# Kernel tuning notes

Measured on AMD Instinct MI355X. Metric: run time of the kernel, lower is better.

The kernel has to match this reference:

```python
import jax, jax.numpy as jnp
import numpy as np

N = 50000
E = 800000
B = 8  # number of graphs


def gcn_conv(x, src, dst, W, b, n_nodes):
    # PyG GCNConv: add self-loops, symmetric deg^{-1/2} normalization,
    # linear transform, scatter-add aggregation at dst, then bias.
    loops = jnp.arange(n_nodes, dtype=src.dtype)
    s = jnp.concatenate([src, loops])
    d = jnp.concatenate([dst, loops])
    deg = jax.ops.segment_sum(jnp.ones_like(d, dtype=x.dtype), d, num_segments=n_nodes)
    dinv = jnp.where(deg > 0, jax.lax.rsqrt(deg), 0.0)
    norm = dinv[s] * dinv[d]                      # [E+N]
    xw = x @ W                                    # [N, out]
    msg = xw[s] * norm[:, None]                   # gather + scale
    out = jax.ops.segment_sum(msg, d, num_segments=n_nodes)  # scatter-add
    return out + b


def global_attention(x, batch, gate_w, gate_b, n_graphs):
    gate = x @ gate_w + gate_b                    # [N, 1]
    gmax = jax.ops.segment_max(gate, batch, num_segments=n_graphs)
    gmax = jnp.where(jnp.isfinite(gmax), gmax, 0.0)
    e = jnp.exp(gate - gmax[batch])               # segment-stable softmax
    denom = jax.ops.segment_sum(e, batch, num_segments=n_graphs)
    alpha = e / denom[batch]                      # [N, 1]
    return jax.ops.segment_sum(alpha * x, batch, num_segments=n_graphs)  # [B, d]


def setup_inputs() -> dict:
    key = jax.random.key(0)
    ks = jax.random.split(key, 10)
    x = jax.random.normal(ks[0], (N, 512), dtype=jnp.float32)
    edge_index = jax.random.randint(ks[1], (2, E), 0, N, dtype=jnp.int32)
    batch = jnp.sort(jax.random.randint(ks[2], (N,), 0, B, dtype=jnp.int32))
    W1 = jax.random.normal(ks[3], (512, 256), dtype=jnp.float32) / np.sqrt(512)
    b1 = jnp.zeros((256,), dtype=jnp.float32)
    W2 = jax.random.normal(ks[4], (256, 256), dtype=jnp.float32) / np.sqrt(256)
    b2 = jnp.zeros((256,), dtype=jnp.float32)
    gate_w = jax.random.normal(ks[5], (256, 1), dtype=jnp.float32) / np.sqrt(256)
    gate_b = jnp.zeros((1,), dtype=jnp.float32)
    return {"x": x, "edge_index": edge_index, "batch": batch,
            "W1": W1, "b1": b1, "W2": W2, "b2": b2,
            "gate_w": gate_w, "gate_b": gate_b}


def reference(x, edge_index, batch, W1, b1, W2, b2, gate_w, gate_b):
    src, dst = edge_index[0], edge_index[1]
    h = jax.nn.relu(gcn_conv(x, src, dst, W1, b1, N))
    h = jax.nn.relu(gcn_conv(h, src, dst, W2, b2, N))
    return global_attention(h, batch, gate_w, gate_b, B)
```

## Files before the change

kernel.cpp:

```cpp
#include <hip/hip_runtime.h>
#include <hip/hip_bf16.h>
#include <math.h>

#define FDIM 256
#define CAP 64
#define NGRAPH 8
#define GMAX_BLOCKS 64
#define FINAL_BLOCKS 512

typedef __attribute__((ext_vector_type(8))) short bf16x8;
typedef __attribute__((ext_vector_type(4))) float f32x4;

__device__ __forceinline__ unsigned enc_f(float x){
  unsigned u = __float_as_uint(x);
  return (u >> 31) ? ~u : (u | 0x80000000u);
}
__device__ __forceinline__ float dec_f(unsigned u){
  return (u >> 31) ? __uint_as_float(u & 0x7FFFFFFFu) : __uint_as_float(~u);
}

__device__ __forceinline__ unsigned short f2bf(float f){
  unsigned u = __float_as_uint(f);
  unsigned r = (u + 0x7FFFu + ((u >> 16) & 1u)) >> 16;
  return (unsigned short)r;
}
__device__ __forceinline__ float bf2f(unsigned short h){
  return __uint_as_float(((unsigned)h) << 16);
}
__device__ __forceinline__ unsigned pk2(float a, float b){
  return (unsigned)f2bf(a) | ((unsigned)f2bf(b) << 16);
}

__global__ void init_k(int* cnt, float* denom, float* out, int N){
  int i = blockIdx.x * blockDim.x + threadIdx.x;
  if (i < N) cnt[i] = 0;
  if (i < NGRAPH) denom[i] = 0.f;
  if (i < NGRAPH * FDIM) out[i] = 0.f;
}

__global__ void csr_k(const int* __restrict__ src, const int* __restrict__ dst,
                      int* __restrict__ cnt, int* __restrict__ col, int E){
  int e = blockIdx.x * blockDim.x + threadIdx.x;
  if (e < E){
    int d = dst[e];
    int pos = atomicAdd(&cnt[d], 1);
    if (pos < CAP) col[(size_t)d * CAP + pos] = src[e];
  }
}

__global__ void dinv_k(const int* __restrict__ cnt, float* __restrict__ dinv, int N){
  int i = blockIdx.x * blockDim.x + threadIdx.x;
  if (i < N) dinv[i] = rsqrtf((float)(cnt[i] + 1));
}

template<int K>
__global__ void wconv_k(const float* __restrict__ W, unsigned short* __restrict__ Wt){
  int idx = blockIdx.x * 256 + threadIdx.x;
  if (idx >= K * 256) return;
  int k = idx >> 8, n = idx & 255;
  Wt[(size_t)n * K + k] = f2bf(W[idx]);
}

template<int K, bool A_FP32>
__global__ __launch_bounds__(512) void gemm_k(const void* __restrict__ Av,
                                              const unsigned short* __restrict__ Bt,
                                              unsigned short* __restrict__ C, int M){
  __shared__ unsigned short As[128 * 64];
  __shared__ unsigned short Bs[256 * 64];
  const int tid = threadIdx.x;
  const int lane = tid & 63, wid = tid >> 6;
  const int wr = wid >> 2, wc = wid & 3;
  const int m0 = blockIdx.x * 128;
  f32x4 acc[4][4] = {};

  float4 arf0, arf1, arf2, arf3;
  uint4  arb0, arb1;
  uint4  brg0, brg1, brg2, brg3;

  const int rA0 = tid >> 3,          kqA0 = tid & 7;
  const int rA1 = (512 + tid) >> 3,  kqA1 = tid & 7;

  auto issue = [&](int k0){
    if (A_FP32){
      const float* A = (const float*)Av;
      const float* p0 = A + (size_t)min(m0 + rA0, M - 1) * K + k0 + kqA0 * 8;
      const float* p1 = A + (size_t)min(m0 + rA1, M - 1) * K + k0 + kqA1 * 8;
      arf0 = *(const float4*)p0; arf1 = *(const float4*)(p0 + 4);
      arf2 = *(const float4*)p1; arf3 = *(const float4*)(p1 + 4);
    } else {
      const unsigned short* A = (const unsigned short*)Av;
      arb0 = *(const uint4*)(A + (size_t)min(m0 + rA0, M - 1) * K + k0 + kqA0 * 8);
      arb1 = *(const uint4*)(A + (size_t)min(m0 + rA1, M - 1) * K + k0 + kqA1 * 8);
    }
    {
      int n0 = tid >> 3, n1 = (512 + tid) >> 3, n2 = (1024 + tid) >> 3, n3 = (1536 + tid) >> 3;
      int kq = tid & 7;
      brg0 = *(const uint4*)(Bt + (size_t)n0 * K + k0 + kq * 8);
      brg1 = *(const uint4*)(Bt + (size_t)n1 * K + k0 + kq * 8);
      brg2 = *(const uint4*)(Bt + (size_t)n2 * K + k0 + kq * 8);
      brg3 = *(const uint4*)(Bt + (size_t)n3 * K + k0 + kq * 8);
    }
  };

  auto writeLDS = [&](){
    int kq = tid & 7;
    {
      uint4 u0, u1;
      if (A_FP32){
        u0.x = pk2(arf0.x, arf0.y); u0.y = pk2(arf0.z, arf0.w);
        u0.z = pk2(arf1.x, arf1.y); u0.w = pk2(arf1.z, arf1.w);
        u1.x = pk2(arf2.x, arf2.y); u1.y = pk2(arf2.z, arf2.w);
        u1.z = pk2(arf3.x, arf3.y); u1.w = pk2(arf3.z, arf3.w);
      } else { u0 = arb0; u1 = arb1; }
      *(uint4*)((char*)As + ((rA0 * 128 + kq * 16) ^ ((rA0 & 7) << 4))) = u0;
      *(uint4*)((char*)As + ((rA1 * 128 + kq * 16) ^ ((rA1 & 7) << 4))) = u1;
    }
    {
      int n0 = tid >> 3, n1 = (512 + tid) >> 3, n2 = (1024 + tid) >> 3, n3 = (1536 + tid) >> 3;
      *(uint4*)((char*)Bs + ((n0 * 128 + kq * 16) ^ ((n0 & 7) << 4))) = brg0;
      *(uint4*)((char*)Bs + ((n1 * 128 + kq * 16) ^ ((n1 & 7) << 4))) = brg1;
      *(uint4*)((char*)Bs + ((n2 * 128 + kq * 16) ^ ((n2 & 7) << 4))) = brg2;
      *(uint4*)((char*)Bs + ((n3 * 128 + kq * 16) ^ ((n3 & 7) << 4))) = brg3;
    }
  };

  issue(0);
  for (int k0 = 0; k0 < K; k0 += 64){
    writeLDS();
    __syncthreads();
    if (k0 + 64 < K) issue(k0 + 64);

    #pragma unroll
    for (int kk = 0; kk < 64; kk += 32){
      bf16x8 af[4], bfr[4];
      int kb = kk * 2 + ((lane >> 4) << 4);
      #pragma unroll
      for (int mi = 0; mi < 4; ++mi){
        int r = wr * 64 + mi * 16 + (lane & 15);
        af[mi] = *(bf16x8*)((char*)As + ((r * 128 + kb) ^ ((r & 7) << 4)));
      }
      #pragma unroll
      for (int ni = 0; ni < 4; ++ni){
        int n = wc * 64 + ni * 16 + (lane & 15);
        bfr[ni] = *(bf16x8*)((char*)Bs + ((n * 128 + kb) ^ ((n & 7) << 4)));
      }
      #pragma unroll
      for (int mi = 0; mi < 4; ++mi)
        #pragma unroll
        for (int ni = 0; ni < 4; ++ni)
          acc[mi][ni] = __builtin_amdgcn_mfma_f32_16x16x32_bf16(af[mi], bfr[ni], acc[mi][ni], 0, 0, 0);
    }
    __syncthreads();
  }

  #pragma unroll
  for (int mi = 0; mi < 4; ++mi){
    #pragma unroll
    for (int reg = 0; reg < 4; ++reg){
      int row = m0 + wr * 64 + mi * 16 + ((lane >> 4) << 2) + reg;
      if (row < M){
        #pragma unroll
        for (int ni = 0; ni < 4; ++ni){
          int colc = wc * 64 + ni * 16 + (lane & 15);
          C[(size_t)row * FDIM + colc] = f2bf(acc[mi][ni][reg]);
        }
      }
    }
  }
}

template<bool OUT_BF16, bool GATE>
__global__ __launch_bounds__(64) void agg_k(const unsigned short* __restrict__ xw,
                                            const float* __restrict__ dinv,
                                            const int* __restrict__ col,
                                            const int* __restrict__ cnt,
                                            const float* __restrict__ bias,
                                            void* __restrict__ outv,
                                            const float* __restrict__ gw,
                                            const float* __restrict__ gb,
                                            float* __restrict__ gate, int N){
  int i = blockIdx.x;
  int lane = threadIdx.x;
  float di = dinv[i];
  int n = min(cnt[i], CAP);
  int s = 0; float w = 0.f;
  if (lane < n){ s = col[(size_t)i * CAP + lane]; w = di * dinv[s]; }

  float a0, a1, a2, a3;
  {
    ushort4 v = *(const ushort4*)(xw + (size_t)i * FDIM + lane * 4);
    float sw = di * di;
    a0 = sw * bf2f(v.x); a1 = sw * bf2f(v.y); a2 = sw * bf2f(v.z); a3 = sw * bf2f(v.w);
  }

  uint2 bufA[8], bufB[8];
  int nc = (n + 7) >> 3;

  auto loadChunk = [&](uint2 (&buf)[8], int c){
    #pragma unroll
    for (int j = 0; j < 8; ++j){
      int e = c * 8 + j;
      int se = __shfl(s, e);
      buf[j] = *(const uint2*)(xw + (size_t)se * FDIM + lane * 4);
    }
  };
  auto consChunk = [&](uint2 (&buf)[8], int c){
    #pragma unroll
    for (int j = 0; j < 8; ++j){
      int e = c * 8 + j;
      float we = __shfl(w, e);
      ushort4 v = *(ushort4*)&buf[j];
      a0 += we * bf2f(v.x); a1 += we * bf2f(v.y);
      a2 += we * bf2f(v.z); a3 += we * bf2f(v.w);
    }
  };

  if (nc > 0) loadChunk(bufA, 0);
  for (int c = 0; c < nc; ++c){
    if (c & 1){
      if (c + 1 < nc) loadChunk(bufA, c + 1);
      consChunk(bufB, c);
    } else {
      if (c + 1 < nc) loadChunk(bufB, c + 1);
      consChunk(bufA, c);
    }
  }

  float4 bv = *(const float4*)(bias + lane * 4);
  a0 = fmaxf(a0 + bv.x, 0.f); a1 = fmaxf(a1 + bv.y, 0.f);
  a2 = fmaxf(a2 + bv.z, 0.f); a3 = fmaxf(a3 + bv.w, 0.f);
  if (OUT_BF16){
    ushort4 r = make_ushort4(f2bf(a0), f2bf(a1), f2bf(a2), f2bf(a3));
    *(ushort4*)((unsigned short*)outv + (size_t)i * FDIM + lane * 4) = r;
  } else {
    *(float4*)((float*)outv + (size_t)i * FDIM + lane * 4) = make_float4(a0, a1, a2, a3);
  }
  if (GATE){
    float4 g = *(const float4*)(gw + lane * 4);
    float val = a0 * g.x + a1 * g.y + a2 * g.z + a3 * g.w;
    #pragma unroll
    for (int off = 32; off; off >>= 1) val += __shfl_down(val, off);
    if (lane == 0) gate[i] = val + gb[0];
  }
}

__global__ __launch_bounds__(256) void gmax_k(const float* __restrict__ gate,
                                              const int* __restrict__ batch,
                                              unsigned* __restrict__ pmax, int N){
  __shared__ unsigned smax[NGRAPH];
  int tid = threadIdx.x;
  if (tid < NGRAPH) smax[tid] = 0u;
  __syncthreads();
  int chunk = (N + gridDim.x - 1) / gridDim.x;
  int begin = blockIdx.x * chunk;
  int end = min(begin + chunk, N);
  int curg = -1; unsigned curm = 0u;
  for (int i = begin + tid; i < end; i += 256){
    int g = batch[i];
    unsigned v = enc_f(gate[i]);
    if (g != curg){
      if (curg >= 0) atomicMax(&smax[curg], curm);
      curg = g; curm = v;
    } else if (v > curm) curm = v;
  }
  if (curg >= 0) atomicMax(&smax[curg], curm);
  __syncthreads();
  if (tid < NGRAPH) pmax[blockIdx.x * NGRAPH + tid] = smax[tid];
}

__global__ __launch_bounds__(256) void denom_k(float* __restrict__ gate,
                                               const int* __restrict__ batch,
                                               const unsigned* __restrict__ pmax,
                                               float* __restrict__ denom, int N){
  __shared__ unsigned sge[NGRAPH];
  __shared__ float gm[NGRAPH];
  __shared__ float dsum[NGRAPH];
  int tid = threadIdx.x;
  if (tid < NGRAPH){ sge[tid] = 0u; dsum[tid] = 0.f; }
  __syncthreads();
  for (int j = tid; j < GMAX_BLOCKS * NGRAPH; j += 256)
    atomicMax(&sge[j & (NGRAPH - 1)], pmax[j]);
  __syncthreads();
  if (tid < NGRAPH){
    unsigned u = sge[tid];
    gm[tid] = (u == 0u) ? 0.f : dec_f(u);
  }
  __syncthreads();
  int chunk = (N + gridDim.x - 1) / gridDim.x;
  int begin = blockIdx.x * chunk;
  int end = min(begin + chunk, N);
  int curg = -1; float cursum = 0.f;
  for (int i = begin + tid; i < end; i += 256){
    int g = batch[i];
    float e = expf(gate[i] - gm[g]);
    gate[i] = e;
    if (g != curg){
      if (curg >= 0) atomicAdd(&dsum[curg], cursum);
      curg = g; cursum = e;
    } else cursum += e;
  }
  if (curg >= 0) atomicAdd(&dsum[curg], cursum);
  __syncthreads();
  if (tid < NGRAPH && dsum[tid] != 0.f) atomicAdd(&denom[tid], dsum[tid]);
}

__global__ __launch_bounds__(256) void final_k(const float* __restrict__ h,
                                               const float* __restrict__ e,
                                               const int* __restrict__ batch,
                                               const float* __restrict__ denom,
                                               float* __restrict__ out, int N){
  __shared__ float sacc[NGRAPH * FDIM];
  int tid = threadIdx.x;
  #pragma unroll
  for (int j = tid; j < NGRAPH * FDIM; j += 256) sacc[j] = 0.f;
  __syncthreads();
  int lane = tid & 63, w = tid >> 6;
  int chunk = (N + gridDim.x - 1) / gridDim.x;
  int begin = blockIdx.x * chunk;
  int end = min(begin + chunk, N);
  float4 acc = make_float4(0.f, 0.f, 0.f, 0.f);
  int curg = -1;
  for (int i = begin + w; i < end; i += 4){
    int g = batch[i];
    if (g != curg){
      if (curg >= 0){
        atomicAdd(&sacc[curg * FDIM + lane * 4 + 0], acc.x);
        atomicAdd(&sacc[curg * FDIM + lane * 4 + 1], acc.y);
        atomicAdd(&sacc[curg * FDIM + lane * 4 + 2], acc.z);
        atomicAdd(&sacc[curg * FDIM + lane * 4 + 3], acc.w);
        acc = make_float4(0.f, 0.f, 0.f, 0.f);
      }
      curg = g;
    }
    float alpha = e[i] / denom[g];
    float4 v = *(const float4*)(h + (size_t)i * FDIM + lane * 4);
    acc.x += alpha * v.x; acc.y += alpha * v.y;
    acc.z += alpha * v.z; acc.w += alpha * v.w;
  }
  if (curg >= 0){
    atomicAdd(&sacc[curg * FDIM + lane * 4 + 0], acc.x);
    atomicAdd(&sacc[curg * FDIM + lane * 4 + 1], acc.y);
    atomicAdd(&sacc[curg * FDIM + lane * 4 + 2], acc.z);
    atomicAdd(&sacc[curg * FDIM + lane * 4 + 3], acc.w);
  }
  __syncthreads();
  if (begin < end){
    int g0 = batch[begin], g1 = batch[end - 1];
    for (int g = g0; g <= g1; ++g){
      float v = sacc[g * FDIM + tid];
      if (v != 0.f) atomicAdd(&out[g * FDIM + tid], v);
    }
  }
}

extern "C" void kernel_launch(void* const* d_in, const int* in_sizes, int n_in,
                              void* d_out, int out_size, void* d_ws, size_t ws_size,
                              hipStream_t stream){
  const float* x     = (const float*)d_in[0];
  const int*   ei    = (const int*)  d_in[1];
  const int*   batch = (const int*)  d_in[2];
  const float* W1    = (const float*)d_in[3];
  const float* b1    = (const float*)d_in[4];
  const float* W2    = (const float*)d_in[5];
  const float* b2    = (const float*)d_in[6];
  const float* gw    = (const float*)d_in[7];
  const float* gb    = (const float*)d_in[8];
  float* out = (float*)d_out;

  const int N = in_sizes[2];
  const int E = in_sizes[1] / 2;
  const int* src = ei;
  const int* dst = ei + E;

  size_t off = 0;
  auto carve = [&](size_t bytes) -> void* {
    void* p = (char*)d_ws + off;
    off += (bytes + 255) / 256 * 256;
    return p;
  };
  float*          h     = (float*)         carve((size_t)N * FDIM * 4);
  unsigned short* h1b   = (unsigned short*)carve((size_t)N * FDIM * 2);
  unsigned short* xwb   = (unsigned short*)carve((size_t)N * FDIM * 2);
  int*            cnt   = (int*)           carve((size_t)N * 4);
  float*          dinv  = (float*)         carve((size_t)N * 4);
  int*            col   = (int*)           carve((size_t)N * CAP * 4);
  float*          gate  = (float*)         carve((size_t)N * 4);
  unsigned*       pmax  = (unsigned*)      carve(GMAX_BLOCKS * NGRAPH * 4);
  float*          denom = (float*)         carve(NGRAPH * 4);
  unsigned short* Wt1   = (unsigned short*)carve((size_t)256 * 512 * 2);
  unsigned short* Wt2   = (unsigned short*)carve((size_t)256 * 256 * 2);
  (void)ws_size; (void)n_in; (void)out_size;

  const int TB = 256;
  init_k<<<(N + TB - 1) / TB, TB, 0, stream>>>(cnt, denom, out, N);
  csr_k<<<(E + TB - 1) / TB, TB, 0, stream>>>(src, dst, cnt, col, E);
  dinv_k<<<(N + TB - 1) / TB, TB, 0, stream>>>(cnt, dinv, N);
  wconv_k<512><<<(512 * 256 + TB - 1) / TB, TB, 0, stream>>>(W1, Wt1);
  wconv_k<256><<<(256 * 256 + TB - 1) / TB, TB, 0, stream>>>(W2, Wt2);

  int gblocks = (N + 127) / 128;
  gemm_k<512, true ><<<gblocks, 512, 0, stream>>>(x,   Wt1, xwb, N);
  agg_k<true,  false><<<N, 64, 0, stream>>>(xwb, dinv, col, cnt, b1, h1b, nullptr, nullptr, nullptr, N);
  gemm_k<256, false><<<gblocks, 512, 0, stream>>>(h1b, Wt2, xwb, N);
  agg_k<false, true ><<<N, 64, 0, stream>>>(xwb, dinv, col, cnt, b2, h, gw, gb, gate, N);

  gmax_k<<<GMAX_BLOCKS, 256, 0, stream>>>(gate, batch, pmax, N);
  denom_k<<<GMAX_BLOCKS, 256, 0, stream>>>(gate, batch, pmax, denom, N);
  final_k<<<FINAL_BLOCKS, 256, 0, stream>>>(h, gate, batch, denom, out, N);
}
```

Baseline: 255.7 us.

## Pack four nodes per block and split edges across half-waves with 16-byte gathers

The aggregation kernel now runs four nodes per 256-thread block instead of one node per 64-thread block. Within each wave, the two 32-lane halves process alternate neighbors, and each lane loads 8 bf16 values (16 bytes) per neighbor instead of 4. The two halves' partial sums are combined with a cross-half shuffle, and the gate dot-product reduction is adjusted to match. The aim is wider memory transactions, fewer blocks to schedule and more gathers in flight per lane. The cost is more accumulator registers and an extra shuffle reduction per node.

```diff
diff --git a/kernel.cpp b/kernel.cpp
--- a/kernel.cpp
+++ b/kernel.cpp
@@ -30,6 +30,8 @@
 __device__ __forceinline__ unsigned pk2(float a, float b){
   return (unsigned)f2bf(a) | ((unsigned)f2bf(b) << 16);
 }
+__device__ __forceinline__ float bfu_lo(unsigned u){ return __uint_as_float(u << 16); }
+__device__ __forceinline__ float bfu_hi(unsigned u){ return __uint_as_float(u & 0xFFFF0000u); }
 
 __global__ void init_k(int* cnt, float* denom, float* out, int N){
   int i = blockIdx.x * blockDim.x + threadIdx.x;
@@ -170,48 +172,58 @@
 }
 
 template<bool OUT_BF16, bool GATE>
-__global__ __launch_bounds__(64) void agg_k(const unsigned short* __restrict__ xw,
-                                            const float* __restrict__ dinv,
-                                            const int* __restrict__ col,
-                                            const int* __restrict__ cnt,
-                                            const float* __restrict__ bias,
-                                            void* __restrict__ outv,
-                                            const float* __restrict__ gw,
-                                            const float* __restrict__ gb,
-                                            float* __restrict__ gate, int N){
-  int i = blockIdx.x;
-  int lane = threadIdx.x;
-  float di = dinv[i];
-  int n = min(cnt[i], CAP);
+__global__ __launch_bounds__(256) void agg_k(const unsigned short* __restrict__ xw,
+                                             const float* __restrict__ dinv,
+                                             const int* __restrict__ col,
+                                             const int* __restrict__ cnt,
+                                             const float* __restrict__ bias,
+                                             void* __restrict__ outv,
+                                             const float* __restrict__ gw,
+                                             const float* __restrict__ gb,
+                                             float* __restrict__ gate, int N){
+  int node = blockIdx.x * 4 + (threadIdx.x >> 6);
+  if (node >= N) return;
+  int lane = threadIdx.x & 63;
+  int half = lane >> 5;
+  int hl = lane & 31;
+
+  float di = dinv[node];
+  int n = min(cnt[node], CAP);
   int s = 0; float w = 0.f;
-  if (lane < n){ s = col[(size_t)i * CAP + lane]; w = di * dinv[s]; }
-
-  float a0, a1, a2, a3;
-  {
-    ushort4 v = *(const ushort4*)(xw + (size_t)i * FDIM + lane * 4);
+  if (lane < n){ s = col[(size_t)node * CAP + lane]; w = di * dinv[s]; }
+
+  float a0=0.f,a1=0.f,a2=0.f,a3=0.f,a4=0.f,a5=0.f,a6=0.f,a7=0.f;
+  if (half == 0){
+    uint4 v = *(const uint4*)(xw + (size_t)node * FDIM + hl * 8);
     float sw = di * di;
-    a0 = sw * bf2f(v.x); a1 = sw * bf2f(v.y); a2 = sw * bf2f(v.z); a3 = sw * bf2f(v.w);
-  }
-
-  uint2 bufA[8], bufB[8];
-  int nc = (n + 7) >> 3;
-
-  auto loadChunk = [&](uint2 (&buf)[8], int c){
+    a0 = sw * bfu_lo(v.x); a1 = sw * bfu_hi(v.x);
+    a2 = sw * bfu_lo(v.y); a3 = sw * bfu_hi(v.y);
+    a4 = sw * bfu_lo(v.z); a5 = sw * bfu_hi(v.z);
+    a6 = sw * bfu_lo(v.w); a7 = sw * bfu_hi(v.w);
+  }
+
+  uint4 bufA[4], bufB[4];
+  int ns = (n + 1) >> 1;
+  int nc = (ns + 3) >> 2;
+
+  auto loadChunk = [&](uint4 (&buf)[4], int c){
     #pragma unroll
-    for (int j = 0; j < 8; ++j){
-      int e = c * 8 + j;
+    for (int j = 0; j < 4; ++j){
+      int e = (c * 4 + j) * 2 + half;
       int se = __shfl(s, e);
-      buf[j] = *(const uint2*)(xw + (size_t)se * FDIM + lane * 4);
+      buf[j] = *(const uint4*)(xw + (size_t)se * FDIM + hl * 8);
     }
   };
-  auto consChunk = [&](uint2 (&buf)[8], int c){
+  auto consChunk = [&](uint4 (&buf)[4], int c){
     #pragma unroll
-    for (int j = 0; j < 8; ++j){
-      int e = c * 8 + j;
+    for (int j = 0; j < 4; ++j){
+      int e = (c * 4 + j) * 2 + half;
       float we = __shfl(w, e);
-      ushort4 v = *(ushort4*)&buf[j];
-      a0 += we * bf2f(v.x); a1 += we * bf2f(v.y);
-      a2 += we * bf2f(v.z); a3 += we * bf2f(v.w);
+      uint4 v = buf[j];
+      a0 += we * bfu_lo(v.x); a1 += we * bfu_hi(v.x);
+      a2 += we * bfu_lo(v.y); a3 += we * bfu_hi(v.y);
+      a4 += we * bfu_lo(v.z); a5 += we * bfu_hi(v.z);
+      a6 += we * bfu_lo(v.w); a7 += we * bfu_hi(v.w);
     }
   };
 
@@ -226,21 +238,38 @@
     }
   }
 
-  float4 bv = *(const float4*)(bias + lane * 4);
-  a0 = fmaxf(a0 + bv.x, 0.f); a1 = fmaxf(a1 + bv.y, 0.f);
-  a2 = fmaxf(a2 + bv.z, 0.f); a3 = fmaxf(a3 + bv.w, 0.f);
-  if (OUT_BF16){
-    ushort4 r = make_ushort4(f2bf(a0), f2bf(a1), f2bf(a2), f2bf(a3));
-    *(ushort4*)((unsigned short*)outv + (size_t)i * FDIM + lane * 4) = r;
-  } else {
-    *(float4*)((float*)outv + (size_t)i * FDIM + lane * 4) = make_float4(a0, a1, a2, a3);
+  a0 += __shfl_xor(a0, 32); a1 += __shfl_xor(a1, 32);
+  a2 += __shfl_xor(a2, 32); a3 += __shfl_xor(a3, 32);
+  a4 += __shfl_xor(a4, 32); a5 += __shfl_xor(a5, 32);
+  a6 += __shfl_xor(a6, 32); a7 += __shfl_xor(a7, 32);
+
+  float4 bv0 = *(const float4*)(bias + hl * 8);
+  float4 bv1 = *(const float4*)(bias + hl * 8 + 4);
+  a0 = fmaxf(a0 + bv0.x, 0.f); a1 = fmaxf(a1 + bv0.y, 0.f);
+  a2 = fmaxf(a2 + bv0.z, 0.f); a3 = fmaxf(a3 + bv0.w, 0.f);
+  a4 = fmaxf(a4 + bv1.x, 0.f); a5 = fmaxf(a5 + bv1.y, 0.f);
+  a6 = fmaxf(a6 + bv1.z, 0.f); a7 = fmaxf(a7 + bv1.w, 0.f);
+
+  if (half == 0){
+    if (OUT_BF16){
+      uint4 r;
+      r.x = pk2(a0, a1); r.y = pk2(a2, a3);
+      r.z = pk2(a4, a5); r.w = pk2(a6, a7);
+      *(uint4*)((unsigned short*)outv + (size_t)node * FDIM + hl * 8) = r;
+    } else {
+      float* po = (float*)outv + (size_t)node * FDIM + hl * 8;
+      *(float4*)po       = make_float4(a0, a1, a2, a3);
+      *(float4*)(po + 4) = make_float4(a4, a5, a6, a7);
+    }
   }
   if (GATE){
-    float4 g = *(const float4*)(gw + lane * 4);
-    float val = a0 * g.x + a1 * g.y + a2 * g.z + a3 * g.w;
+    float4 g0 = *(const float4*)(gw + hl * 8);
+    float4 g1 = *(const float4*)(gw + hl * 8 + 4);
+    float val = a0*g0.x + a1*g0.y + a2*g0.z + a3*g0.w
+              + a4*g1.x + a5*g1.y + a6*g1.z + a7*g1.w;
     #pragma unroll
-    for (int off = 32; off; off >>= 1) val += __shfl_down(val, off);
-    if (lane == 0) gate[i] = val + gb[0];
+    for (int off = 16; off; off >>= 1) val += __shfl_xor(val, off);
+    if (lane == 0) gate[node] = val + gb[0];
   }
 }
 
@@ -399,10 +428,11 @@
   wconv_k<256><<<(256 * 256 + TB - 1) / TB, TB, 0, stream>>>(W2, Wt2);
 
   int gblocks = (N + 127) / 128;
+  int ablocks = (N + 3) / 4;
   gemm_k<512, true ><<<gblocks, 512, 0, stream>>>(x,   Wt1, xwb, N);
-  agg_k<true,  false><<<N, 64, 0, stream>>>(xwb, dinv, col, cnt, b1, h1b, nullptr, nullptr, nullptr, N);
+  agg_k<true,  false><<<ablocks, 256, 0, stream>>>(xwb, dinv, col, cnt, b1, h1b, nullptr, nullptr, nullptr, N);
   gemm_k<256, false><<<gblocks, 512, 0, stream>>>(h1b, Wt2, xwb, N);
-  agg_k<false, true ><<<N, 64, 0, stream>>>(xwb, dinv, col, cnt, b2, h, gw, gb, gate, N);
+  agg_k<false, true ><<<ablocks, 256, 0, stream>>>(xwb, dinv, col, cnt, b2, h, gw, gb, gate, N);
 
   gmax_k<<<GMAX_BLOCKS, 256, 0, stream>>>(gate, batch, pmax, N);
   denom_k<<<GMAX_BLOCKS, 256, 0, stream>>>(gate, batch, pmax, denom, N);
```

New measurement: 265.4 us. 1.04x slower.
